# Kernel tuning notes

Hardware: AMD Instinct MI355X
Metric: run time of the kernel (lower is better)

The kernel has to match this reference:

```python
import jax, jax.numpy as jnp
import numpy as np

DIM_MODEL = 1024
NUM_HEADS = 16
DROPOUT_P = 0.5
SCALE = float(np.sqrt(DIM_MODEL // NUM_HEADS))  # NOTE: source MULTIPLIES by this (unusual but faithful)
DROP_KEY = jax.random.key(42)


def setup_inputs() -> dict:
    key = jax.random.key(0)
    ks = jax.random.split(key, 9)
    B, LQ, LK, D = 4, 2048, 2048, DIM_MODEL
    s = 1.0 / np.sqrt(D)
    return {
        "query": jax.random.normal(ks[0], (B, LQ, D), jnp.float32),
        "key": jax.random.normal(ks[1], (B, LK, D), jnp.float32),
        "value": jax.random.normal(ks[2], (B, LK, D), jnp.float32),
        "Wq": jax.random.normal(ks[3], (D, D), jnp.float32) * s,
        "bq": jax.random.normal(ks[4], (D,), jnp.float32) * s,
        "Wk": jax.random.normal(ks[5], (D, D), jnp.float32) * s,
        "bk": jax.random.normal(ks[6], (D,), jnp.float32) * s,
        "Wv": jax.random.normal(ks[7], (D, D), jnp.float32) * s,
        "bv": jax.random.normal(ks[8], (D,), jnp.float32) * s,
    }


def reference(query, key, value, Wq, bq, Wk, bk, Wv, bv):
    # Linear projections (W stored as [in, out])
    q = jnp.einsum('bqd,de->bqe', query, Wq) + bq
    k = jnp.einsum('bkd,de->bke', key, Wk) + bk
    v = jnp.einsum('bkd,de->bke', value, Wv) + bv
    # scores scaled by MULTIPLYING sqrt(d_head), per source
    scores = jnp.einsum('bqe,bke->bqk', q, k) * SCALE
    probs = jax.nn.softmax(scores, axis=-1)
    # dropout (train mode, p=0.5), deterministic fixed key for reproducibility
    keep = jax.random.bernoulli(DROP_KEY, 1.0 - DROPOUT_P, probs.shape)
    probs = jnp.where(keep, probs / (1.0 - DROPOUT_P), 0.0)
    return jnp.einsum('bqk,bke->bqe', probs, v)
```

## Files before the change

kernel.cpp:

```cpp
#include <hip/hip_runtime.h>
#include <math.h>

#define BATCH  4
#define LSEQ   2048
#define DMODEL 1024
#define MROWS  (BATCH * LSEQ)
#define SCORE_SCALE 8.0f

#define THREEFRY_PARTITIONABLE 1

typedef __bf16 bf16_t;
typedef bf16_t bf16x8 __attribute__((ext_vector_type(8)));
typedef bf16_t bf16x4 __attribute__((ext_vector_type(4)));
typedef float  f32x4  __attribute__((ext_vector_type(4)));

#define LDSP(p) ((__attribute__((address_space(3))) void*)(p))
#define GLBP(p) ((const __attribute__((address_space(1))) void*)(p))

__device__ __forceinline__ unsigned rotl32(unsigned x, int r) {
    return (x << r) | (x >> (32 - r));
}

__device__ __forceinline__ void threefry2x32(unsigned k0, unsigned k1,
                                             unsigned x0, unsigned x1,
                                             unsigned& o0, unsigned& o1) {
    const unsigned ks0 = k0, ks1 = k1, ks2 = k0 ^ k1 ^ 0x1BD11BDAu;
    x0 += ks0; x1 += ks1;
#define TF_R(r) { x0 += x1; x1 = rotl32(x1, r); x1 ^= x0; }
    TF_R(13) TF_R(15) TF_R(26) TF_R(6)
    x0 += ks1; x1 += ks2 + 1u;
    TF_R(17) TF_R(29) TF_R(16) TF_R(24)
    x0 += ks2; x1 += ks0 + 2u;
    TF_R(13) TF_R(15) TF_R(26) TF_R(6)
    x0 += ks0; x1 += ks1 + 3u;
    TF_R(17) TF_R(29) TF_R(16) TF_R(24)
    x0 += ks1; x1 += ks2 + 4u;
    TF_R(13) TF_R(15) TF_R(26) TF_R(6)
    x0 += ks2; x1 += ks0 + 5u;
#undef TF_R
    o0 = x0; o1 = x1;
}

__device__ __forceinline__ bool dropout_keep(unsigned n) {
    unsigned o0, o1;
#if THREEFRY_PARTITIONABLE
    threefry2x32(0u, 42u, 0u, n, o0, o1);
    unsigned bits = o0 ^ o1;
#else
    const unsigned HALF = (unsigned)(BATCH * LSEQ) * (unsigned)LSEQ / 2u;
    unsigned c0 = (n < HALF) ? n : (n - HALF);
    unsigned c1 = (n < HALF) ? (n + HALF) : n;
    threefry2x32(0u, 42u, c0, c1, o0, o1);
    unsigned bits = (n < HALF) ? o0 : o1;
#endif
    return bits < 0x80000000u;
}

__global__ __launch_bounds__(256)
void split_f32(const float* __restrict__ X0, const float* __restrict__ X1,
               bf16_t* __restrict__ hi, bf16_t* __restrict__ lo, int n) {
    const int y = blockIdx.y;
    const float* X = y ? X1 : X0;
    long long i = (long long)(blockIdx.x * 256 + threadIdx.x) * 4;
    if (i >= n) return;
    float4 v = *(const float4*)(X + i);
    bf16x4 h, l;
    h[0] = (bf16_t)v.x; l[0] = (bf16_t)(v.x - (float)h[0]);
    h[1] = (bf16_t)v.y; l[1] = (bf16_t)(v.y - (float)h[1]);
    h[2] = (bf16_t)v.z; l[2] = (bf16_t)(v.z - (float)h[2]);
    h[3] = (bf16_t)v.w; l[3] = (bf16_t)(v.w - (float)h[3]);
    *(bf16x4*)(hi + (long long)y * n + i) = h;
    *(bf16x4*)(lo + (long long)y * n + i) = l;
}

__global__ __launch_bounds__(256)
void cvt_bf16(const float* __restrict__ X, bf16_t* __restrict__ Y, int n) {
    long long i = (long long)(blockIdx.x * 256 + threadIdx.x) * 8;
    if (i >= n) return;
    float4 a = *(const float4*)(X + i);
    float4 b = *(const float4*)(X + i + 4);
    bf16x8 o;
    o[0] = (bf16_t)a.x; o[1] = (bf16_t)a.y; o[2] = (bf16_t)a.z; o[3] = (bf16_t)a.w;
    o[4] = (bf16_t)b.x; o[5] = (bf16_t)b.y; o[6] = (bf16_t)b.z; o[7] = (bf16_t)b.w;
    *(bf16x8*)(Y + i) = o;
}

__global__ __launch_bounds__(256)
void split_transpose(const float* __restrict__ W0, const float* __restrict__ W1,
                     bf16_t* __restrict__ Th, bf16_t* __restrict__ Tl,
                     int Kd, int Nd) {
    __shared__ float t[32][33];
    const int z = blockIdx.z;
    const float* W = z ? W1 : W0;
    const long long zo = (long long)z * Kd * Nd;
    const int bx = blockIdx.x * 32;
    const int by = blockIdx.y * 32;
    const int tx = threadIdx.x & 31, ty = threadIdx.x >> 5;
#pragma unroll
    for (int i = 0; i < 4; ++i)
        t[ty + i * 8][tx] = W[(long long)(by + ty + i * 8) * Nd + bx + tx];
    __syncthreads();
#pragma unroll
    for (int i = 0; i < 4; ++i) {
        float v = t[tx][ty + i * 8];
        long long idx = zo + (long long)(bx + ty + i * 8) * Kd + by + tx;
        bf16_t h = (bf16_t)v;
        Th[idx] = h;
        Tl[idx] = (bf16_t)(v - (float)h);
    }
}

template <int SPLIT, int OUT, int BROW>
__global__ __launch_bounds__(256)
void gemm_mfma(const bf16_t* __restrict__ Ah, const bf16_t* __restrict__ Al,
               const bf16_t* __restrict__ Bh, const bf16_t* __restrict__ Bl,
               const float* __restrict__ bias, const float* __restrict__ bias2,
               float* __restrict__ Cf, bf16_t* __restrict__ Ch,
               bf16_t* __restrict__ Cl,
               int M, int N, int K, float scale,
               long long sA, long long sB, long long sC,
               int SX, int NYt) {
    constexpr int TM = 128, TN = 128, TOT = 256, CHUNKS = 4;
    constexpr int NB = SPLIT ? 2 : 1;
    constexpr int BUFSZ = NB * TOT * 32;
    __shared__ __align__(16) bf16_t smem[2 * BUFSZ];

    const int bid = blockIdx.x;
    const int xcd = bid & 7;
    const int ii = bid >> 3;
    const int perz = SX * NYt;
    const int zz = ii / perz;
    const int rr = ii - zz * perz;
    const int nx = xcd + ((rr % SX) << 3);
    const int my = rr / SX;
    const long long z = zz;
    const int m0 = my * TM, n0 = nx * TN;

    const int tid = threadIdx.x;
    const int lane = tid & 63;
    const int wave = tid >> 6;
    const int quad = lane >> 4;
    const int l16 = lane & 15;
    const int wm = (wave & 1) * 64;
    const int wn = (wave >> 1) * 64;

    const bf16_t* gAh = Ah + z * sA;
    const bf16_t* gBh = Bh + z * sB;
    const bf16_t* gAl = SPLIT ? Al + z * sA : nullptr;
    const bf16_t* gBl = SPLIT ? Bl + z * sB : nullptr;

    const int lrow = lane >> 2;
    const int scol = ((lane & 3) ^ ((lrow >> 1) & 3)) * 8;
    const int sw = (l16 >> 1) & 3;

    auto issue = [&](int k0, int b) {
        bf16_t* base = smem + b * BUFSZ;
#pragma unroll
        for (int c = 0; c < CHUNKS; ++c) {
            const int rbase = wave * 64 + c * 16;
            const int row = rbase + lrow;
            if (rbase < TM) {
                const long long g = (long long)(m0 + row) * K + k0 + scol;
                __builtin_amdgcn_global_load_lds(GLBP(gAh + g), LDSP(base + row * 32), 16, 0, 0);
                if constexpr (SPLIT)
                    __builtin_amdgcn_global_load_lds(GLBP(gAl + g), LDSP(base + TOT * 32 + row * 32), 16, 0, 0);
            } else {
                const int br = row - TM;
                const long long g = (long long)(n0 + br) * K + k0 + scol;
                __builtin_amdgcn_global_load_lds(GLBP(gBh + g), LDSP(base + TM * 32 + br * 32), 16, 0, 0);
                if constexpr (SPLIT)
                    __builtin_amdgcn_global_load_lds(GLBP(gBl + g), LDSP(base + TOT * 32 + TM * 32 + br * 32), 16, 0, 0);
            }
        }
    };

    f32x4 acc[4][4];
#pragma unroll
    for (int i = 0; i < 4; ++i)
#pragma unroll
        for (int j = 0; j < 4; ++j)
            acc[i][j] = (f32x4){0.f, 0.f, 0.f, 0.f};

    issue(0, 0);
    const int NIT = K >> 5;
    for (int it = 0; it < NIT; ++it) {
        const int b = it & 1;
        const bool more = (it + 1) < NIT;
        if (more) issue((it + 1) << 5, b ^ 1);
        if constexpr (SPLIT) {
            if (more) asm volatile("s_waitcnt vmcnt(8)" ::: "memory");
            else      asm volatile("s_waitcnt vmcnt(0)" ::: "memory");
        } else {
            if (more) asm volatile("s_waitcnt vmcnt(4)" ::: "memory");
            else      asm volatile("s_waitcnt vmcnt(0)" ::: "memory");
        }
        asm volatile("s_barrier" ::: "memory");

        bf16_t* base = smem + b * BUFSZ;
        bf16_t* sAh = base;
        bf16_t* sBh = base + TM * 32;
        bf16_t* sAl = base + TOT * 32;
        bf16_t* sBl = base + TOT * 32 + TM * 32;

        bf16x8 afh[4], bfh[4], afl[4], bfl[4];
#pragma unroll
        for (int i = 0; i < 4; ++i) {
            const int ao = (wm + i * 16 + l16) * 32 + (quad ^ sw) * 8;
            afh[i] = *(const bf16x8*)(sAh + ao);
            if constexpr (SPLIT) afl[i] = *(const bf16x8*)(sAl + ao);
        }
#pragma unroll
        for (int j = 0; j < 4; ++j) {
            const int bo = (wn + j * 16 + l16) * 32 + (quad ^ sw) * 8;
            bfh[j] = *(const bf16x8*)(sBh + bo);
            if constexpr (SPLIT) bfl[j] = *(const bf16x8*)(sBl + bo);
        }
#pragma unroll
        for (int i = 0; i < 4; ++i)
#pragma unroll
            for (int j = 0; j < 4; ++j) {
                acc[i][j] = __builtin_amdgcn_mfma_f32_16x16x32_bf16(afh[i], bfh[j], acc[i][j], 0, 0, 0);
                if constexpr (SPLIT) {
                    acc[i][j] = __builtin_amdgcn_mfma_f32_16x16x32_bf16(afh[i], bfl[j], acc[i][j], 0, 0, 0);
                    acc[i][j] = __builtin_amdgcn_mfma_f32_16x16x32_bf16(afl[i], bfh[j], acc[i][j], 0, 0, 0);
                }
            }
        asm volatile("s_barrier" ::: "memory");
    }

    const float* bz = (z == 1 && bias2) ? bias2 : bias;
#pragma unroll
    for (int i = 0; i < 4; ++i)
#pragma unroll
        for (int j = 0; j < 4; ++j) {
            const int n = n0 + wn + j * 16 + l16;
            float bvn = 0.f;
            if constexpr (OUT != 0 && !BROW) bvn = bz[n];
#pragma unroll
            for (int r = 0; r < 4; ++r) {
                const int m = m0 + wm + i * 16 + quad * 4 + r;
                const long long idx = z * sC + (long long)m * N + n;
                float v = acc[i][j][r];
                if constexpr (OUT == 0) {
                    Cf[idx] = v * scale;
                } else if constexpr (OUT == 1) {
                    v += bvn;
                    bf16_t h = (bf16_t)v;
                    Ch[idx] = h;
                    Cl[idx] = (bf16_t)(v - (float)h);
                } else {
                    v += BROW ? bz[m] : bvn;
                    Ch[idx] = (bf16_t)v;
                }
            }
        }
}

template <int OUT>
__global__ __launch_bounds__(512, 2)
void gemm_mfma_8ph(const bf16_t* __restrict__ Ah, const bf16_t* __restrict__ Al,
                   const bf16_t* __restrict__ Bh, const bf16_t* __restrict__ Bl,
                   const float* __restrict__ bias, const float* __restrict__ bias2,
                   float* __restrict__ Cf, bf16_t* __restrict__ Ch,
                   bf16_t* __restrict__ Cl,
                   int M, int N, int K, float scale,
                   long long sA, long long sB, long long sC,
                   int NYt, int NZ) {
    constexpr int TM = 256, TN = 256;
    constexpr int PLANE = 256 * 32;
    constexpr int HB = 4 * PLANE;
    __shared__ __align__(16) bf16_t smem[2 * HB];

    const int bid = blockIdx.x;
    const int gid = (bid & 7) * 32 + (bid >> 3);
    const int nzy = NZ * NYt;
    const int nx = gid / nzy;
    const int rem = gid - nx * nzy;
    const int zz = rem / NYt;
    const int my = rem - zz * NYt;
    const long long z = zz;
    const int m0 = my * TM, n0 = nx * TN;

    const int tid = threadIdx.x;
    const int lane = tid & 63;
    const int wave = tid >> 6;
    const int quad = lane >> 4;
    const int l16 = lane & 15;
    const int wm = (wave >> 2) * 128;
    const int wn = (wave & 3) * 64;

    const bf16_t* gAh = Ah + z * sA;
    const bf16_t* gAl = Al + z * sA;
    const bf16_t* gBh = Bh + z * sB;
    const bf16_t* gBl = Bl + z * sB;

    const int lrow = lane >> 2;
    const int scol = ((lane & 3) ^ ((lrow >> 1) & 3)) * 8;
    const int sw = (l16 >> 1) & 3;

    auto stage_round = [&](int r, int k0, bf16_t* base) {
        if (r < 4) {
            const int row = ((r & 1) << 7) + (wave << 4) + lrow;
            const bf16_t* src = (r >= 2) ? gBl : gBh;
            bf16_t* dst = base + ((r >= 2) ? 3 : 2) * PLANE + row * 32;
            __builtin_amdgcn_global_load_lds(
                GLBP(src + (long long)(n0 + row) * K + k0 + scol), LDSP(dst), 16, 0, 0);
        } else {
            const int p = r - 4;
            const int row = (p << 5) + ((wave & 2) ? 128 : 0) + ((wave & 1) << 4) + lrow;
            const bf16_t* src = (wave >= 4) ? gAl : gAh;
            bf16_t* dst = base + ((wave >= 4) ? 1 : 0) * PLANE + row * 32;
            __builtin_amdgcn_global_load_lds(
                GLBP(src + (long long)(m0 + row) * K + k0 + scol), LDSP(dst), 16, 0, 0);
        }
    };

    f32x4 acc[8][4];
#pragma unroll
    for (int i = 0; i < 8; ++i)
#pragma unroll
        for (int j = 0; j < 4; ++j)
            acc[i][j] = (f32x4){0.f, 0.f, 0.f, 0.f};

    bf16x8 ah[2][2], al[2][2];
    bf16x8 bfh[4], bfl[4];

#pragma unroll
    for (int r = 0; r < 8; ++r) stage_round(r, 0, smem);
    asm volatile("s_waitcnt vmcnt(2)" ::: "memory");
    asm volatile("s_barrier" ::: "memory");
    __builtin_amdgcn_sched_barrier(0);
#pragma unroll
    for (int i = 0; i < 2; ++i) {
        const int ao = (wm + i * 16 + l16) * 32 + (quad ^ sw) * 8;
        ah[0][i] = *(const bf16x8*)(smem + ao);
        al[0][i] = *(const bf16x8*)(smem + PLANE + ao);
    }
#pragma unroll
    for (int j = 0; j < 4; ++j) {
        const int bo = (wn + j * 16 + l16) * 32 + (quad ^ sw) * 8;
        bfh[j] = *(const bf16x8*)(smem + 2 * PLANE + bo);
        bfl[j] = *(const bf16x8*)(smem + 3 * PLANE + bo);
    }

    const int NIT = K >> 5;
    for (int itp = 0; itp < NIT; itp += 2) {
#pragma unroll
        for (int h = 0; h < 2; ++h) {
            const int it = itp + h;
            const bool more = (it + 1) < NIT;
            const int k1 = (it + 1) << 5;
            bf16_t* cur = smem + h * HB;
            bf16_t* nxt = smem + (h ^ 1) * HB;
#pragma unroll
            for (int ph = 0; ph < 4; ++ph) {
                if (ph < 3) {
#pragma unroll
                    for (int i = 0; i < 2; ++i) {
                        const int ao = (wm + ((ph + 1) * 2 + i) * 16 + l16) * 32 + (quad ^ sw) * 8;
                        ah[(ph + 1) & 1][i] = *(const bf16x8*)(cur + ao);
                        al[(ph + 1) & 1][i] = *(const bf16x8*)(cur + PLANE + ao);
                    }
                } else if (more) {
#pragma unroll
                    for (int i = 0; i < 2; ++i) {
                        const int ao = (wm + i * 16 + l16) * 32 + (quad ^ sw) * 8;
                        ah[0][i] = *(const bf16x8*)(nxt + ao);
                        al[0][i] = *(const bf16x8*)(nxt + PLANE + ao);
                    }
                }
                if (more) {
                    if (ph == 0)      { stage_round(0, k1, nxt); stage_round(1, k1, nxt); stage_round(2, k1, nxt); }
                    else if (ph == 1) { stage_round(3, k1, nxt); stage_round(4, k1, nxt); }
                    else if (ph == 2) { stage_round(5, k1, nxt); stage_round(6, k1, nxt); }
                    else              { stage_round(7, k1, nxt); }
                }
                __builtin_amdgcn_s_setprio(1);
#pragma unroll
                for (int i = 0; i < 2; ++i)
#pragma unroll
                    for (int j = 0; j < 4; ++j) {
                        f32x4 a = acc[ph * 2 + i][j];
                        a = __builtin_amdgcn_mfma_f32_16x16x32_bf16(ah[ph & 1][i], bfh[j], a, 0, 0, 0);
                        a = __builtin_amdgcn_mfma_f32_16x16x32_bf16(ah[ph & 1][i], bfl[j], a, 0, 0, 0);
                        a = __builtin_amdgcn_mfma_f32_16x16x32_bf16(al[ph & 1][i], bfh[j], a, 0, 0, 0);
                        acc[ph * 2 + i][j] = a;
                    }
                __builtin_amdgcn_s_setprio(0);
                if (ph == 3 && more) {
#pragma unroll
                    for (int j = 0; j < 4; ++j) {
                        const int bo = (wn + j * 16 + l16) * 32 + (quad ^ sw) * 8;
                        bfh[j] = *(const bf16x8*)(nxt + 2 * PLANE + bo);
                        bfl[j] = *(const bf16x8*)(nxt + 3 * PLANE + bo);
                    }
                }
                if (more) {
                    if (ph == 0)      asm volatile("s_waitcnt vmcnt(4)" ::: "memory");
                    else if (ph == 1) asm volatile("s_waitcnt vmcnt(5)" ::: "memory");
                    else              asm volatile("s_waitcnt vmcnt(2)" ::: "memory");
                    asm volatile("s_barrier" ::: "memory");
                    __builtin_amdgcn_sched_barrier(0);
                } else {
                    if (ph == 0) {
                        asm volatile("s_waitcnt vmcnt(1)" ::: "memory");
                        asm volatile("s_barrier" ::: "memory");
                        __builtin_amdgcn_sched_barrier(0);
                    } else if (ph == 1) {
                        asm volatile("s_waitcnt vmcnt(0)" ::: "memory");
                        asm volatile("s_barrier" ::: "memory");
                        __builtin_amdgcn_sched_barrier(0);
                    }
                }
            }
        }
    }

    const float* bz = (z == 1 && bias2) ? bias2 : bias;
#pragma unroll
    for (int i = 0; i < 8; ++i)
#pragma unroll
        for (int j = 0; j < 4; ++j) {
            const int n = n0 + wn + j * 16 + l16;
            float bvn = 0.f;
            if constexpr (OUT != 0) bvn = bz[n];
#pragma unroll
            for (int r = 0; r < 4; ++r) {
                const int m = m0 + wm + i * 16 + quad * 4 + r;
                const long long idx = z * sC + (long long)m * N + n;
                float v = acc[i][j][r];
                if constexpr (OUT == 0) {
                    Cf[idx] = v * scale;
                } else {
                    v += bvn;
                    bf16_t h = (bf16_t)v;
                    Ch[idx] = h;
                    Cl[idx] = (bf16_t)(v - (float)h);
                }
            }
        }
}

__global__ __launch_bounds__(256)
void softmax_dropout(const float* __restrict__ S, bf16_t* __restrict__ P) {
    const unsigned row = blockIdx.x;
    const float* rp = S + (long long)row * LSEQ;
    const int tid = threadIdx.x;

    float v[8];
    *(float4*)(v)     = *(const float4*)(rp + tid * 8);
    *(float4*)(v + 4) = *(const float4*)(rp + tid * 8 + 4);

    float m = v[0];
#pragma unroll
    for (int e = 1; e < 8; ++e) m = fmaxf(m, v[e]);
#pragma unroll
    for (int o = 1; o < 64; o <<= 1) m = fmaxf(m, __shfl_xor(m, o));
    __shared__ float redm[4];
    if ((tid & 63) == 0) redm[tid >> 6] = m;
    __syncthreads();
    m = fmaxf(fmaxf(redm[0], redm[1]), fmaxf(redm[2], redm[3]));

    float s = 0.f;
#pragma unroll
    for (int e = 0; e < 8; ++e) { v[e] = __expf(v[e] - m); s += v[e]; }
#pragma unroll
    for (int o = 1; o < 64; o <<= 1) s += __shfl_xor(s, o);
    __shared__ float reds[4];
    if ((tid & 63) == 0) reds[tid >> 6] = s;
    __syncthreads();
    s = (reds[0] + reds[1]) + (reds[2] + reds[3]);

    const float inv = 2.0f / s;
    const unsigned nb = row * (unsigned)LSEQ + (unsigned)(tid * 8);
    bf16x8 o8;
#pragma unroll
    for (int e = 0; e < 8; ++e)
        o8[e] = (bf16_t)(dropout_keep(nb + e) ? v[e] * inv : 0.0f);
    *(bf16x8*)(P + (long long)row * LSEQ + tid * 8) = o8;
}

extern "C" void kernel_launch(void* const* d_in, const int* in_sizes, int n_in,
                              void* d_out, int out_size, void* d_ws, size_t ws_size,
                              hipStream_t stream) {
    const float* query = (const float*)d_in[0];
    const float* key_  = (const float*)d_in[1];
    const float* value = (const float*)d_in[2];
    const float* Wq = (const float*)d_in[3];
    const float* bq = (const float*)d_in[4];
    const float* Wk = (const float*)d_in[5];
    const float* bk = (const float*)d_in[6];
    const float* Wv = (const float*)d_in[7];
    const float* bv = (const float*)d_in[8];
    float* out = (float*)d_out;

    char* w = (char*)d_ws;
    const size_t Q1 = (size_t)MROWS * DMODEL * 2;
    bf16_t* Qh  = (bf16_t*)(w);
    bf16_t* Ql  = (bf16_t*)(w + 2 * Q1);
    bf16_t* VT  = (bf16_t*)(w + 4 * Q1);
    float*  S   = (float*)(w + 5 * Q1);
    bf16_t* XvH  = (bf16_t*)(w + 5 * Q1);
    bf16_t* XqkH = (bf16_t*)(w + 5 * Q1);
    bf16_t* XqkL = (bf16_t*)(w + 7 * Q1);
    bf16_t* WTh = (bf16_t*)(w + 9 * Q1);
    bf16_t* WTl = (bf16_t*)(w + 9 * Q1 + 2 * (size_t)DMODEL * DMODEL * 2);
    bf16_t* P   = Qh;

    dim3 b256(256);
    dim3 b512(512);
    const int NELEM = MROWS * DMODEL;
    const long long DD = (long long)DMODEL * DMODEL;
    dim3 gwt1(DMODEL / 32, DMODEL / 32, 1);
    dim3 gwt2(DMODEL / 32, DMODEL / 32, 2);

    split_transpose<<<gwt1, b256, 0, stream>>>(Wv, nullptr, WTh, WTl, DMODEL, DMODEL);
    cvt_bf16<<<dim3(NELEM / 2048), b256, 0, stream>>>(value, XvH, NELEM);
    gemm_mfma<0, 2, 1><<<dim3(512), b256, 0, stream>>>(
        WTh, nullptr, XvH, nullptr, bv, nullptr, nullptr, VT, nullptr,
        DMODEL, LSEQ, DMODEL, 1.f,
        0, (long long)LSEQ * DMODEL, (long long)DMODEL * LSEQ,
        2, DMODEL / 128);

    split_transpose<<<gwt2, b256, 0, stream>>>(Wq, Wk, WTh, WTl, DMODEL, DMODEL);
    split_f32<<<dim3(NELEM / 1024, 2), b256, 0, stream>>>(query, key_, XqkH, XqkL, NELEM);
    gemm_mfma_8ph<1><<<dim3(256), b512, 0, stream>>>(
        XqkH, XqkL, WTh, WTl, bq, bk, nullptr, Qh, Ql,
        MROWS, DMODEL, DMODEL, 1.f,
        (long long)NELEM, DD, (long long)NELEM,
        MROWS / 256, 2);

    gemm_mfma_8ph<0><<<dim3(256), b512, 0, stream>>>(
        Qh, Ql, Qh + NELEM, Ql + NELEM, nullptr, nullptr, S, nullptr, nullptr,
        LSEQ, LSEQ, DMODEL, SCORE_SCALE,
        (long long)LSEQ * DMODEL, (long long)LSEQ * DMODEL,
        (long long)LSEQ * LSEQ,
        LSEQ / 256, 4);

    softmax_dropout<<<dim3(MROWS), b256, 0, stream>>>(S, P);

    gemm_mfma<0, 0, 0><<<dim3(512), b256, 0, stream>>>(
        P, nullptr, VT, nullptr, nullptr, nullptr, out, nullptr, nullptr,
        LSEQ, DMODEL, LSEQ, 1.f,
        (long long)LSEQ * LSEQ, (long long)DMODEL * LSEQ,
        (long long)LSEQ * DMODEL,
        1, LSEQ / 128);
}
```

Measured before the change: 437.6 us.

## Replace 128x128 GEMM with 512-thread triple-buffered 128x256 pipelined kernel

Replaces the generic double-buffered 128x128 bf16 MFMA GEMM used for the V projection and the P·V product with a 512-thread kernel on 128x256 tiles. It keeps a three-stage LDS ring and prefetches the next k-step's fragments into registers while the current MFMAs run, raising MFMA priority with s_setprio. It also remaps block IDs across XCDs. The aim is to hide global-to-LDS latency and cut per-iteration barrier stalls, at the cost of more LDS and registers per block and a hard-coded grid mapping that assumes 256 blocks.

```diff
diff --git a/kernel.cpp b/kernel.cpp
--- a/kernel.cpp
+++ b/kernel.cpp
@@ -110,67 +110,56 @@
     }
 }
 
-template <int SPLIT, int OUT, int BROW>
-__global__ __launch_bounds__(256)
-void gemm_mfma(const bf16_t* __restrict__ Ah, const bf16_t* __restrict__ Al,
-               const bf16_t* __restrict__ Bh, const bf16_t* __restrict__ Bl,
-               const float* __restrict__ bias, const float* __restrict__ bias2,
+template <int OUT>
+__global__ __launch_bounds__(512, 2)
+void gemm_pipe(const bf16_t* __restrict__ A, const bf16_t* __restrict__ B,
+               const float* __restrict__ bias,
                float* __restrict__ Cf, bf16_t* __restrict__ Ch,
-               bf16_t* __restrict__ Cl,
                int M, int N, int K, float scale,
                long long sA, long long sB, long long sC,
-               int SX, int NYt) {
-    constexpr int TM = 128, TN = 128, TOT = 256, CHUNKS = 4;
-    constexpr int NB = SPLIT ? 2 : 1;
-    constexpr int BUFSZ = NB * TOT * 32;
-    __shared__ __align__(16) bf16_t smem[2 * BUFSZ];
+               int NYt, int NZ) {
+    constexpr int ABUF = 128 * 32;
+    constexpr int BUFE = ABUF + 256 * 32;
+    __shared__ __align__(16) bf16_t smem[3 * BUFE];
 
     const int bid = blockIdx.x;
-    const int xcd = bid & 7;
-    const int ii = bid >> 3;
-    const int perz = SX * NYt;
-    const int zz = ii / perz;
-    const int rr = ii - zz * perz;
-    const int nx = xcd + ((rr % SX) << 3);
-    const int my = rr / SX;
+    const int gid = (bid & 7) * 32 + (bid >> 3);
+    const int nzy = NZ * NYt;
+    const int nx = gid / nzy;
+    const int rem = gid - nx * nzy;
+    const int zz = rem / NYt;
+    const int my = rem - zz * NYt;
     const long long z = zz;
-    const int m0 = my * TM, n0 = nx * TN;
+    const int m0 = my * 128, n0 = nx * 256;
 
     const int tid = threadIdx.x;
     const int lane = tid & 63;
     const int wave = tid >> 6;
     const int quad = lane >> 4;
     const int l16 = lane & 15;
-    const int wm = (wave & 1) * 64;
-    const int wn = (wave >> 1) * 64;
-
-    const bf16_t* gAh = Ah + z * sA;
-    const bf16_t* gBh = Bh + z * sB;
-    const bf16_t* gAl = SPLIT ? Al + z * sA : nullptr;
-    const bf16_t* gBl = SPLIT ? Bl + z * sB : nullptr;
+    const int wm = (wave >> 2) * 64;
+    const int wn = (wave & 3) * 64;
+
+    const bf16_t* gA = A + z * sA;
+    const bf16_t* gB = B + z * sB;
 
     const int lrow = lane >> 2;
     const int scol = ((lane & 3) ^ ((lrow >> 1) & 3)) * 8;
     const int sw = (l16 >> 1) & 3;
 
-    auto issue = [&](int k0, int b) {
-        bf16_t* base = smem + b * BUFSZ;
-#pragma unroll
-        for (int c = 0; c < CHUNKS; ++c) {
-            const int rbase = wave * 64 + c * 16;
-            const int row = rbase + lrow;
-            if (rbase < TM) {
-                const long long g = (long long)(m0 + row) * K + k0 + scol;
-                __builtin_amdgcn_global_load_lds(GLBP(gAh + g), LDSP(base + row * 32), 16, 0, 0);
-                if constexpr (SPLIT)
-                    __builtin_amdgcn_global_load_lds(GLBP(gAl + g), LDSP(base + TOT * 32 + row * 32), 16, 0, 0);
-            } else {
-                const int br = row - TM;
-                const long long g = (long long)(n0 + br) * K + k0 + scol;
-                __builtin_amdgcn_global_load_lds(GLBP(gBh + g), LDSP(base + TM * 32 + br * 32), 16, 0, 0);
-                if constexpr (SPLIT)
-                    __builtin_amdgcn_global_load_lds(GLBP(gBl + g), LDSP(base + TOT * 32 + TM * 32 + br * 32), 16, 0, 0);
-            }
+    auto stage_tile = [&](int k0, bf16_t* base) {
+        {
+            const int row = (wave << 4) + lrow;
+            __builtin_amdgcn_global_load_lds(
+                GLBP(gA + (long long)(m0 + row) * K + k0 + scol),
+                LDSP(base + row * 32), 16, 0, 0);
+        }
+#pragma unroll
+        for (int r = 0; r < 2; ++r) {
+            const int row = (r << 7) + (wave << 4) + lrow;
+            __builtin_amdgcn_global_load_lds(
+                GLBP(gB + (long long)(n0 + row) * K + k0 + scol),
+                LDSP(base + ABUF + row * 32), 16, 0, 0);
         }
     };
 
@@ -181,61 +170,76 @@
         for (int j = 0; j < 4; ++j)
             acc[i][j] = (f32x4){0.f, 0.f, 0.f, 0.f};
 
-    issue(0, 0);
+    bf16x8 fa0[4], fb0[4], fa1[4], fb1[4];
+
     const int NIT = K >> 5;
-    for (int it = 0; it < NIT; ++it) {
-        const int b = it & 1;
-        const bool more = (it + 1) < NIT;
-        if (more) issue((it + 1) << 5, b ^ 1);
-        if constexpr (SPLIT) {
-            if (more) asm volatile("s_waitcnt vmcnt(8)" ::: "memory");
-            else      asm volatile("s_waitcnt vmcnt(0)" ::: "memory");
-        } else {
-            if (more) asm volatile("s_waitcnt vmcnt(4)" ::: "memory");
-            else      asm volatile("s_waitcnt vmcnt(0)" ::: "memory");
-        }
-        asm volatile("s_barrier" ::: "memory");
-
-        bf16_t* base = smem + b * BUFSZ;
-        bf16_t* sAh = base;
-        bf16_t* sBh = base + TM * 32;
-        bf16_t* sAl = base + TOT * 32;
-        bf16_t* sBl = base + TOT * 32 + TM * 32;
-
-        bf16x8 afh[4], bfh[4], afl[4], bfl[4];
-#pragma unroll
-        for (int i = 0; i < 4; ++i) {
-            const int ao = (wm + i * 16 + l16) * 32 + (quad ^ sw) * 8;
-            afh[i] = *(const bf16x8*)(sAh + ao);
-            if constexpr (SPLIT) afl[i] = *(const bf16x8*)(sAl + ao);
-        }
-#pragma unroll
-        for (int j = 0; j < 4; ++j) {
-            const int bo = (wn + j * 16 + l16) * 32 + (quad ^ sw) * 8;
-            bfh[j] = *(const bf16x8*)(sBh + bo);
-            if constexpr (SPLIT) bfl[j] = *(const bf16x8*)(sBl + bo);
-        }
-#pragma unroll
-        for (int i = 0; i < 4; ++i)
-#pragma unroll
-            for (int j = 0; j < 4; ++j) {
-                acc[i][j] = __builtin_amdgcn_mfma_f32_16x16x32_bf16(afh[i], bfh[j], acc[i][j], 0, 0, 0);
-                if constexpr (SPLIT) {
-                    acc[i][j] = __builtin_amdgcn_mfma_f32_16x16x32_bf16(afh[i], bfl[j], acc[i][j], 0, 0, 0);
-                    acc[i][j] = __builtin_amdgcn_mfma_f32_16x16x32_bf16(afl[i], bfh[j], acc[i][j], 0, 0, 0);
-                }
-            }
-        asm volatile("s_barrier" ::: "memory");
-    }
-
-    const float* bz = (z == 1 && bias2) ? bias2 : bias;
+
+    bf16_t* p0 = smem;
+    bf16_t* p1 = smem + BUFE;
+    bf16_t* p2 = smem + 2 * BUFE;
+
+    stage_tile(0, p0);
+    stage_tile(32, p1);
+    stage_tile(64, p2);
+    asm volatile("s_waitcnt vmcnt(3)" ::: "memory");
+    asm volatile("s_barrier" ::: "memory");
+    __builtin_amdgcn_sched_barrier(0);
+#pragma unroll
+    for (int i = 0; i < 4; ++i) {
+        const int ao = (wm + i * 16 + l16) * 32 + (quad ^ sw) * 8;
+        fa0[i] = *(const bf16x8*)(p0 + ao);
+    }
+#pragma unroll
+    for (int j = 0; j < 4; ++j) {
+        const int bo = ABUF + (wn + j * 16 + l16) * 32 + (quad ^ sw) * 8;
+        fb0[j] = *(const bf16x8*)(p0 + bo);
+    }
+
+#define PIPE_ITER(T, FAc, FBc, FAn, FBn)                                      \
+    {                                                                         \
+        const int t_ = (T);                                                   \
+        if (t_ + 1 < NIT) {                                                   \
+            _Pragma("unroll")                                                 \
+            for (int i = 0; i < 4; ++i) {                                     \
+                const int ao = (wm + i * 16 + l16) * 32 + (quad ^ sw) * 8;    \
+                FAn[i] = *(const bf16x8*)(p1 + ao);                           \
+            }                                                                 \
+            _Pragma("unroll")                                                 \
+            for (int j = 0; j < 4; ++j) {                                     \
+                const int bo = ABUF + (wn + j * 16 + l16) * 32 + (quad ^ sw) * 8; \
+                FBn[j] = *(const bf16x8*)(p1 + bo);                           \
+            }                                                                 \
+        }                                                                     \
+        if (t_ + 3 < NIT) stage_tile((t_ + 3) << 5, p0);                      \
+        __builtin_amdgcn_s_setprio(1);                                        \
+        _Pragma("unroll")                                                     \
+        for (int i = 0; i < 4; ++i)                                           \
+            _Pragma("unroll")                                                 \
+            for (int j = 0; j < 4; ++j)                                       \
+                acc[i][j] = __builtin_amdgcn_mfma_f32_16x16x32_bf16(          \
+                    FAc[i], FBc[j], acc[i][j], 0, 0, 0);                      \
+        __builtin_amdgcn_s_setprio(0);                                        \
+        if (t_ + 2 < NIT) {                                                   \
+            asm volatile("s_waitcnt lgkmcnt(0)" ::: "memory");                \
+            if (t_ + 3 < NIT) asm volatile("s_waitcnt vmcnt(3)" ::: "memory");\
+            else              asm volatile("s_waitcnt vmcnt(0)" ::: "memory");\
+            asm volatile("s_barrier" ::: "memory");                           \
+            __builtin_amdgcn_sched_barrier(0);                                \
+        }                                                                     \
+        { bf16_t* tmp_ = p0; p0 = p1; p1 = p2; p2 = tmp_; }                   \
+    }
+
+    for (int tp = 0; tp < NIT; tp += 2) {
+        PIPE_ITER(tp,     fa0, fb0, fa1, fb1)
+        PIPE_ITER(tp + 1, fa1, fb1, fa0, fb0)
+    }
+#undef PIPE_ITER
+
 #pragma unroll
     for (int i = 0; i < 4; ++i)
 #pragma unroll
         for (int j = 0; j < 4; ++j) {
             const int n = n0 + wn + j * 16 + l16;
-            float bvn = 0.f;
-            if constexpr (OUT != 0 && !BROW) bvn = bz[n];
 #pragma unroll
             for (int r = 0; r < 4; ++r) {
                 const int m = m0 + wm + i * 16 + quad * 4 + r;
@@ -243,14 +247,8 @@
                 float v = acc[i][j][r];
                 if constexpr (OUT == 0) {
                     Cf[idx] = v * scale;
-                } else if constexpr (OUT == 1) {
-                    v += bvn;
-                    bf16_t h = (bf16_t)v;
-                    Ch[idx] = h;
-                    Cl[idx] = (bf16_t)(v - (float)h);
                 } else {
-                    v += BROW ? bz[m] : bvn;
-                    Ch[idx] = (bf16_t)v;
+                    Ch[idx] = (bf16_t)(v + bias[m]);
                 }
             }
         }
@@ -516,11 +514,11 @@
 
     split_transpose<<<gwt1, b256, 0, stream>>>(Wv, nullptr, WTh, WTl, DMODEL, DMODEL);
     cvt_bf16<<<dim3(NELEM / 2048), b256, 0, stream>>>(value, XvH, NELEM);
-    gemm_mfma<0, 2, 1><<<dim3(512), b256, 0, stream>>>(
-        WTh, nullptr, XvH, nullptr, bv, nullptr, nullptr, VT, nullptr,
+    gemm_pipe<2><<<dim3(256), b512, 0, stream>>>(
+        WTh, XvH, bv, nullptr, VT,
         DMODEL, LSEQ, DMODEL, 1.f,
         0, (long long)LSEQ * DMODEL, (long long)DMODEL * LSEQ,
-        2, DMODEL / 128);
+        DMODEL / 128, 4);
 
     split_transpose<<<gwt2, b256, 0, stream>>>(Wq, Wk, WTh, WTl, DMODEL, DMODEL);
     split_f32<<<dim3(NELEM / 1024, 2), b256, 0, stream>>>(query, key_, XqkH, XqkL, NELEM);
@@ -539,10 +537,9 @@
 
     softmax_dropout<<<dim3(MROWS), b256, 0, stream>>>(S, P);
 
-    gemm_mfma<0, 0, 0><<<dim3(512), b256, 0, stream>>>(
-        P, nullptr, VT, nullptr, nullptr, nullptr, out, nullptr, nullptr,
+    gemm_pipe<0><<<dim3(256), b512, 0, stream>>>(
+        P, VT, nullptr, out, nullptr,
         LSEQ, DMODEL, LSEQ, 1.f,
-        (long long)LSEQ * LSEQ, (long long)DMODEL * LSEQ,
-        (long long)LSEQ * DMODEL,
-        1, LSEQ / 128);
-}
+        (long long)LSEQ * LSEQ, (long long)DMODEL * LSEQ, (long long)LSEQ * DMODEL,
+        LSEQ / 128, 4);
+}
```

After: 425.1 us. 2.9% less time.
